# Performance work log

Measured on AMD Instinct MI355X. Metric: run time of the kernel, lower is better.

Reference implementation:

```python
import jax, jax.numpy as jnp
import numpy as np

H = W = 128; WS = 8; SHIFT = 4; HEADS = 4; T = 2; EPS = 1e-5
N = WS * WS  # tokens per window per frame


def _rel_pos_index(ws):
    ch, cw = np.meshgrid(np.arange(ws), np.arange(ws), indexing='ij')
    coords = np.stack([ch, cw]).reshape(2, -1)  # (2, N)
    rel = coords[:, :, None] - coords[:, None, :]  # (2, N, N)
    rel = rel.transpose(1, 2, 0)
    rel[:, :, 0] += ws - 1
    rel[:, :, 1] += ws - 1
    rel[:, :, 0] *= 2 * ws - 1
    return rel.sum(-1)  # (N, N) int


def _attn_mask(h, w, ws, shift):
    img = np.zeros((h, w))
    cnt = 0
    for hs in (slice(0, -ws), slice(-ws, -shift), slice(-shift, None)):
        for wsl in (slice(0, -ws), slice(-ws, -shift), slice(-shift, None)):
            img[hs, wsl] = cnt
            cnt += 1
    mw = img.reshape(h // ws, ws, w // ws, ws).transpose(0, 2, 1, 3).reshape(-1, ws * ws)
    diff = mw[:, None, :] - mw[:, :, None]
    return np.where(diff != 0, -100.0, 0.0).astype(np.float32)  # (nW, N, N)


REL_IDX = jnp.asarray(_rel_pos_index(WS))
ATTN_MASK = jnp.asarray(_attn_mask(H, W, WS, SHIFT))


def _ln(x, g, b):
    mu = x.mean(-1, keepdims=True)
    var = ((x - mu) ** 2).mean(-1, keepdims=True)
    return (x - mu) * jax.lax.rsqrt(var + EPS) * g + b


def setup_inputs() -> dict:
    key = jax.random.key(0)
    ks = jax.random.split(key, 8)
    B, C = 4, 128
    hid = 4 * C
    s = 0.02
    return {
        'x_v': jax.random.normal(ks[0], (B, T, H * W, C), jnp.float32),
        'qkv_w': jax.random.normal(ks[1], (3 * C, C), jnp.float32) * s,
        'qkv_b': jnp.zeros((3 * C,), jnp.float32),
        'proj_w': jax.random.normal(ks[2], (C, C), jnp.float32) * s,
        'proj_b': jnp.zeros((C,), jnp.float32),
        'rpb_table': jax.random.normal(ks[3], ((2 * WS - 1) ** 2, HEADS), jnp.float32) * s,
        'norm1_w': jnp.ones((C,), jnp.float32),
        'norm1_b': jnp.zeros((C,), jnp.float32),
        'norm2_w': jnp.ones((C,), jnp.float32),
        'norm2_b': jnp.zeros((C,), jnp.float32),
        'fc1_w': jax.random.normal(ks[4], (hid, C), jnp.float32) * s,
        'fc1_b': jnp.zeros((hid,), jnp.float32),
        'fc2_w': jax.random.normal(ks[5], (C, hid), jnp.float32) * s,
        'fc2_b': jnp.zeros((C,), jnp.float32),
    }


def reference(x_v, qkv_w, qkv_b, proj_w, proj_b, rpb_table,
              norm1_w, norm1_b, norm2_w, norm2_b,
              fc1_w, fc1_b, fc2_w, fc2_b):
    B, Tt, L, C = x_v.shape
    hd = C // HEADS
    nWh, nWw = H // WS, W // WS
    nW = nWh * nWw
    TN = T * N

    shortcut = x_v.reshape(B * T, L, C)
    x = x_v.reshape(B * T, H, W, C)
    x = jnp.roll(x, (-SHIFT, -SHIFT), axis=(1, 2))
    # window partition: (B*T, nWh, ws, nWw, ws, C) -> (B*nW, T, N, C)
    x = x.reshape(B * T, nWh, WS, nWw, WS, C).transpose(0, 1, 3, 2, 4, 5)
    x = x.reshape(B, T, nW, N, C).transpose(0, 2, 1, 3, 4).reshape(B * nW, T, N, C)

    # --- window attention over T*N tokens ---
    B_ = B * nW
    xf = x.reshape(B_, TN, C)
    qkv = xf @ qkv_w.T + qkv_b  # (B_, TN, 3C)
    qkv = qkv.reshape(B_, TN, 3, HEADS, hd).transpose(2, 0, 3, 1, 4)
    q, k, v = qkv[0], qkv[1], qkv[2]  # (B_, heads, TN, hd)
    q = q * (hd ** -0.5)
    attn = jnp.einsum('bhqd,bhkd->bhqk', q, k)  # (B_, heads, TN, TN)

    rpb = rpb_table[REL_IDX.reshape(-1)].reshape(N, N, HEADS).transpose(2, 0, 1)
    rpb = jnp.tile(rpb, (1, T, T))  # (heads, TN, TN)
    attn = attn + rpb[None]

    mask = jnp.tile(ATTN_MASK, (1, T, T))  # (nW, TN, TN)
    attn = attn.reshape(B, nW, HEADS, TN, TN) + mask[None, :, None]
    attn = jax.nn.softmax(attn.reshape(B_, HEADS, TN, TN), axis=-1)

    out = jnp.einsum('bhqk,bhkd->bhqd', attn, v)  # (B_, heads, TN, hd)
    out = out.transpose(0, 2, 1, 3).reshape(B_, T, N, C)
    out = out.reshape(B_ * T * N, C) @ proj_w.T + proj_b
    out = out.reshape(B_, T, N, C)

    # window reverse: (B*nW, T, N, C) -> (B, T, H, W, C)
    x = out.reshape(B, nWh, nWw, T, WS, WS, C).transpose(0, 3, 1, 4, 2, 5, 6)
    x = x.reshape(B * T, H, W, C)
    x = jnp.roll(x, (SHIFT, SHIFT), axis=(1, 2)).reshape(B * T, L, C)

    x = shortcut + x
    h = _ln(x, norm2_w, norm2_b)
    h = jax.nn.gelu(h @ fc1_w.T + fc1_b, approximate=False) @ fc2_w.T + fc2_b
    x = _ln(x + h, norm1_w, norm1_b)
    return x.reshape(B, T, L, C)
```

## Files before the change

kernel.cpp:

```cpp
#include <hip/hip_runtime.h>

typedef unsigned short us;
typedef short s16x8 __attribute__((ext_vector_type(8)));
typedef float f32x4 __attribute__((ext_vector_type(4)));

__device__ __forceinline__ us f2bf(float f) {
  union { float f; unsigned u; } v; v.f = f;
  unsigned u = v.u;
  u += 0x7fffu + ((u >> 16) & 1u);
  return (us)(u >> 16);
}
__device__ __forceinline__ float bf2f(us u) {
  union { unsigned u; float f; } v; v.u = ((unsigned)u) << 16; return v.f;
}
__device__ __forceinline__ s16x8 ld8(const us* p) { return *(const s16x8*)p; }

#define MFMA(a, b, c) __builtin_amdgcn_mfma_f32_16x16x32_bf16(a, b, c, 0, 0, 0)

__device__ __forceinline__ void lds_fence() {
  asm volatile("s_waitcnt lgkmcnt(0)" ::: "memory");
}

__device__ __forceinline__ float qsum(float v) {
  v += __shfl_xor(v, 1, 64); v += __shfl_xor(v, 2, 64);
  v += __shfl_xor(v, 4, 64); v += __shfl_xor(v, 8, 64);
  return v;
}

__device__ __forceinline__ float gelu_fast(float x) {
  float ax = fabsf(x);
  float t = __builtin_amdgcn_rcpf(1.f + 0.3275911f * ax);
  float p = t * (0.254829592f +
            t * (-0.284496736f +
            t * (1.421413741f +
            t * (-1.453152027f +
            t * 1.061405429f))));
  float e = __expf(-ax * ax);
  float er = copysignf(1.f - p * e, x);
  return 0.5f * x * (1.f + er);
}

__global__ void prep_kernel(const float* __restrict__ qkv_w, const float* __restrict__ proj_w,
                            const float* __restrict__ fc1_w, const float* __restrict__ fc2_w,
                            const float* __restrict__ rpb_table,
                            us* __restrict__ qkvw, us* __restrict__ projw,
                            us* __restrict__ fc1w, us* __restrict__ fc2w,
                            us* __restrict__ rpbm) {
  int id = blockIdx.x * 256 + threadIdx.x;
  if (id < 49152) {
    int n = id % 384, k = id / 384;
    float v = qkv_w[n * 128 + k];
    if (n < 128) v *= 0.17677669529663687f;
    qkvw[(((k >> 3) * 384 + n) << 3) + (k & 7)] = f2bf(v);
    return;
  }
  id -= 49152;
  if (id < 16384) { int n = id % 128, k = id / 128;
    projw[(((k >> 3) * 128 + n) << 3) + (k & 7)] = f2bf(proj_w[n * 128 + k]); return; }
  id -= 16384;
  if (id < 65536) { int n = id % 512, k = id / 512;
    fc1w[(((k >> 3) * 512 + n) << 3) + (k & 7)] = f2bf(fc1_w[n * 128 + k]); return; }
  id -= 65536;
  if (id < 65536) { int n = id % 128, k = id / 128;
    fc2w[(((k >> 3) * 128 + n) << 3) + (k & 7)] = f2bf(fc2_w[n * 512 + k]); return; }
  id -= 65536;
  {
    int h = id >> 14, cls = (id >> 12) & 3, e = id & 4095;
    int n1 = e >> 6, n2 = e & 63;
    int r1 = n1 >> 3, c1 = n1 & 7, r2 = n2 >> 3, c2 = n2 & 7;
    int cH = cls >> 1, cW = cls & 1;
    int cq = (cH ? (r1 < 4 ? 1 : 2) : 0) * 3 + (cW ? (c1 < 4 ? 1 : 2) : 0);
    int ck = (cH ? (r2 < 4 ? 1 : 2) : 0) * 3 + (cW ? (c2 < 4 ? 1 : 2) : 0);
    int ridx = (r1 - r2 + 7) * 15 + (c1 - c2 + 7);
    float v = rpb_table[ridx * 4 + h] + (cq != ck ? -100.f : 0.f);
    rpbm[id] = f2bf(v);
  }
}

__global__ __launch_bounds__(512, 2) void qkv_attn_kernel(
    const float* __restrict__ x_v, const us* __restrict__ qkvw,
    const float* __restrict__ qkv_b, const us* __restrict__ rpbm,
    us* __restrict__ attn_out) {
  __shared__ __align__(16) unsigned char smem[139264];
  us* A   = (us*)smem;
  us* Qs  = (us*)smem;
  us* Ks  = (us*)(smem + 34816);
  us* Vts = (us*)(smem + 69632);

  int w = blockIdx.x;
  int b = w >> 8, wi = w & 255, wh = wi >> 4, ww = wi & 15;
  int tid = threadIdx.x;

  {
    int token = tid >> 2, q = tid & 3;
    int t = token >> 6, n = token & 63, r = n >> 3, c = n & 7;
    int hs = (wh * 8 + r + 4) & 127, wsc = (ww * 8 + c + 4) & 127;
    const float* src = x_v + (size_t)((b * 2 + t) * 16384 + hs * 128 + wsc) * 128 + q * 32;
    us* dst = A + token * 136 + q * 32;
#pragma unroll
    for (int i = 0; i < 4; ++i) {
      float4 f0 = ((const float4*)src)[2 * i];
      float4 f1 = ((const float4*)src)[2 * i + 1];
      s16x8 v;
      v[0] = (short)f2bf(f0.x); v[1] = (short)f2bf(f0.y);
      v[2] = (short)f2bf(f0.z); v[3] = (short)f2bf(f0.w);
      v[4] = (short)f2bf(f1.x); v[5] = (short)f2bf(f1.y);
      v[6] = (short)f2bf(f1.z); v[7] = (short)f2bf(f1.w);
      *(s16x8*)(dst + i * 8) = v;
    }
  }
  __syncthreads();

  int lane = tid & 63, wv = tid >> 6, quad = lane >> 4, c16 = lane & 15;
  int h = wv >> 1, p = wv & 1;
  int clsid = ((wh == 15) ? 2 : 0) + ((ww == 15) ? 1 : 0);

  int rb = p * 64;
  f32x4 acc[4][6];
#pragma unroll
  for (int mi = 0; mi < 4; ++mi)
#pragma unroll
    for (int ni = 0; ni < 6; ++ni) acc[mi][ni] = (f32x4){0.f, 0.f, 0.f, 0.f};
#pragma unroll
  for (int ks = 0; ks < 4; ++ks) {
    int k0 = ks * 32;
    s16x8 af[4];
#pragma unroll
    for (int mi = 0; mi < 4; ++mi)
      af[mi] = ld8(A + (rb + mi * 16 + c16) * 136 + k0 + quad * 8);
#pragma unroll
    for (int ni = 0; ni < 6; ++ni) {
      int gcol = (ni >> 1) * 128 + h * 32 + (ni & 1) * 16 + c16;
      s16x8 bf = ld8(qkvw + ((((k0 >> 3) + quad) * 384 + gcol) << 3));
#pragma unroll
      for (int mi = 0; mi < 4; ++mi) acc[mi][ni] = MFMA(af[mi], bf, acc[mi][ni]);
    }
  }
  __syncthreads();
#pragma unroll
  for (int ni = 0; ni < 6; ++ni) {
    int part = ni >> 1, colh = (ni & 1) * 16 + c16;
    int col = h * 32 + colh;
    float bias = qkv_b[part * 128 + col];
    if (part == 0) bias *= 0.17677669529663687f;
#pragma unroll
    for (int mi = 0; mi < 4; ++mi)
#pragma unroll
      for (int r = 0; r < 4; ++r) {
        int tok = rb + mi * 16 + quad * 4 + r;
        us v = f2bf(acc[mi][ni][r] + bias);
        if (part == 0) Qs[tok * 136 + col] = v;
        else if (part == 1) Ks[tok * 136 + col] = v;
        else Vts[col * 136 + tok] = v;
      }
  }
  __syncthreads();

  us* Pw = (us*)(smem + 104448 + wv * 4352);
  const us* rsrc = rpbm + ((h * 4 + clsid) << 12);
  int cb = h * 32;

  for (int qq = 0; qq < 4; ++qq) {
    int q0 = (p * 4 + qq) * 16;
    s16x8 aq = ld8(Qs + (q0 + c16) * 136 + cb + quad * 8);
    float rbv[8][4];
#pragma unroll
    for (int nj = 0; nj < 8; ++nj) {
      int nk = (nj * 16 + c16) & 63;
#pragma unroll
      for (int r = 0; r < 4; ++r) {
        int nq = (q0 + quad * 4 + r) & 63;
        rbv[nj][r] = bf2f(rsrc[nq * 64 + nk]);
      }
    }
    f32x4 sacc[8];
#pragma unroll
    for (int nj = 0; nj < 8; ++nj) {
      s16x8 bk = ld8(Ks + (nj * 16 + c16) * 136 + cb + quad * 8);
      f32x4 z = (f32x4){0.f, 0.f, 0.f, 0.f};
      sacc[nj] = MFMA(aq, bk, z);
    }
    float sm[4] = {0.f, 0.f, 0.f, 0.f};
#pragma unroll
    for (int nj = 0; nj < 8; ++nj)
#pragma unroll
      for (int r = 0; r < 4; ++r) {
        float pp = __expf(sacc[nj][r] + rbv[nj][r]);
        sacc[nj][r] = pp;
        sm[r] += pp;
      }
    float inv[4];
#pragma unroll
    for (int r = 0; r < 4; ++r) inv[r] = 1.f / qsum(sm[r]);
#pragma unroll
    for (int nj = 0; nj < 8; ++nj)
#pragma unroll
      for (int r = 0; r < 4; ++r)
        Pw[(quad * 4 + r) * 136 + nj * 16 + c16] = f2bf(sacc[nj][r] * inv[r]);
    lds_fence();
    f32x4 oacc[2];
    oacc[0] = (f32x4){0.f, 0.f, 0.f, 0.f};
    oacc[1] = (f32x4){0.f, 0.f, 0.f, 0.f};
#pragma unroll
    for (int ks = 0; ks < 4; ++ks) {
      int k0 = ks * 32;
      s16x8 ap = ld8(Pw + c16 * 136 + k0 + quad * 8);
#pragma unroll
      for (int nt = 0; nt < 2; ++nt) {
        s16x8 bv = ld8(Vts + (cb + nt * 16 + c16) * 136 + k0 + quad * 8);
        oacc[nt] = MFMA(ap, bv, oacc[nt]);
      }
    }
#pragma unroll
    for (int nt = 0; nt < 2; ++nt)
#pragma unroll
      for (int r = 0; r < 4; ++r) {
        int tok = q0 + quad * 4 + r;
        attn_out[((size_t)w * 128 + tok) * 128 + cb + nt * 16 + c16] =
            f2bf(oacc[nt][r]);
      }
    lds_fence();
  }
}

__global__ __launch_bounds__(256) void fused_kernel5(
    const us* __restrict__ attn_ws, const us* __restrict__ projw,
    const float* __restrict__ proj_b, const float* __restrict__ x_v,
    const us* __restrict__ fc1w, const us* __restrict__ fc2w,
    const float* __restrict__ fc1_b, const float* __restrict__ fc2_b,
    const float* __restrict__ n2w, const float* __restrict__ n2b,
    const float* __restrict__ n1w, const float* __restrict__ n1b,
    float* __restrict__ out) {
  __shared__ __align__(16) unsigned char smem[26624];
  us* A = (us*)smem;
  int blk = blockIdx.x;
  int w = blk >> 1, hb = (blk & 1) * 64;
  int b = w >> 8, wi = w & 255, wh = wi >> 4, ww = wi & 15;
  int tid = threadIdx.x;
  int lane = tid & 63, wv = tid >> 6, quad = lane >> 4, c16 = lane & 15;
  int r0 = wv * 16;
  us* Hw = (us*)(smem + 17408 + wv * 2304);

  {
    int lr = r0 + (lane >> 2), q = lane & 3;
    const us* src = attn_ws + ((size_t)w * 128 + hb + lr) * 128 + q * 32;
    us* dst = A + lr * 136 + q * 32;
#pragma unroll
    for (int i = 0; i < 4; ++i) *(s16x8*)(dst + i * 8) = ld8(src + i * 8);
  }

  size_t grow[4];
  float xv[4][8];
#pragma unroll
  for (int r = 0; r < 4; ++r) {
    int tt = hb + r0 + quad * 4 + r;
    int t = tt >> 6, n = tt & 63, rr = n >> 3, cc2 = n & 7;
    int hf = (wh * 8 + rr + 4) & 127, wf = (ww * 8 + cc2 + 4) & 127;
    grow[r] = (size_t)((b * 2 + t) * 16384 + hf * 128 + wf) * 128;
#pragma unroll
    for (int ni = 0; ni < 8; ++ni) xv[r][ni] = x_v[grow[r] + ni * 16 + c16];
  }
  lds_fence();

  f32x4 y[8];
#pragma unroll
  for (int ni = 0; ni < 8; ++ni) y[ni] = (f32x4){0.f, 0.f, 0.f, 0.f};
#pragma unroll
  for (int ks = 0; ks < 4; ++ks) {
    int k0 = ks * 32;
    s16x8 af = ld8(A + (r0 + c16) * 136 + k0 + quad * 8);
#pragma unroll
    for (int ni = 0; ni < 8; ++ni) {
      s16x8 bf = ld8(projw + ((((k0 >> 3) + quad) * 128 + ni * 16 + c16) << 3));
      y[ni] = MFMA(af, bf, y[ni]);
    }
  }

  {
    float sum[4] = {0.f, 0.f, 0.f, 0.f}, sq[4] = {0.f, 0.f, 0.f, 0.f};
#pragma unroll
    for (int ni = 0; ni < 8; ++ni) {
      float pb = proj_b[ni * 16 + c16];
#pragma unroll
      for (int r = 0; r < 4; ++r) {
        float v = y[ni][r] + pb + xv[r][ni];
        y[ni][r] = v;
        sum[r] += v; sq[r] += v * v;
      }
    }
#pragma unroll
    for (int r = 0; r < 4; ++r) {
      float s = qsum(sum[r]), q = qsum(sq[r]);
      float mean = s * 0.0078125f;
      float rstd = rsqrtf(q * 0.0078125f - mean * mean + 1e-5f);
      int m = r0 + quad * 4 + r;
#pragma unroll
      for (int ni = 0; ni < 8; ++ni) {
        int col = ni * 16 + c16;
        A[m * 136 + col] = f2bf((y[ni][r] - mean) * rstd * n2w[col] + n2b[col]);
      }
    }
  }
  lds_fence();

  f32x4 o[8];
#pragma unroll
  for (int ni = 0; ni < 8; ++ni) o[ni] = (f32x4){0.f, 0.f, 0.f, 0.f};

#pragma unroll
  for (int cc = 0; cc < 8; ++cc) {
    f32x4 f[4];
#pragma unroll
    for (int ni = 0; ni < 4; ++ni) f[ni] = (f32x4){0.f, 0.f, 0.f, 0.f};
#pragma unroll
    for (int ks = 0; ks < 4; ++ks) {
      int k0 = ks * 32;
      s16x8 af = ld8(A + (r0 + c16) * 136 + k0 + quad * 8);
#pragma unroll
      for (int ni = 0; ni < 4; ++ni) {
        s16x8 bf = ld8(fc1w + ((((k0 >> 3) + quad) * 512 + cc * 64 + ni * 16 + c16) << 3));
        f[ni] = MFMA(af, bf, f[ni]);
      }
    }
#pragma unroll
    for (int ni = 0; ni < 4; ++ni) {
      float bb = fc1_b[cc * 64 + ni * 16 + c16];
#pragma unroll
      for (int r = 0; r < 4; ++r) {
        float u = f[ni][r] + bb;
        Hw[(quad * 4 + r) * 72 + ni * 16 + c16] = f2bf(gelu_fast(u));
      }
    }
    lds_fence();
#pragma unroll
    for (int ks2 = 0; ks2 < 2; ++ks2) {
      s16x8 ah = ld8(Hw + c16 * 72 + ks2 * 32 + quad * 8);
#pragma unroll
      for (int ni = 0; ni < 8; ++ni) {
        s16x8 bf = ld8(fc2w + (((cc * 8 + ks2 * 4 + quad) * 128 + ni * 16 + c16) << 3));
        o[ni] = MFMA(ah, bf, o[ni]);
      }
    }
    lds_fence();
  }

  {
    float s1[4] = {0.f, 0.f, 0.f, 0.f}, q1[4] = {0.f, 0.f, 0.f, 0.f};
#pragma unroll
    for (int ni = 0; ni < 8; ++ni) {
      float fb = fc2_b[ni * 16 + c16];
#pragma unroll
      for (int r = 0; r < 4; ++r) {
        float v = o[ni][r] + fb + y[ni][r];
        y[ni][r] = v;
        s1[r] += v; q1[r] += v * v;
      }
    }
#pragma unroll
    for (int r = 0; r < 4; ++r) {
      float s = qsum(s1[r]), q = qsum(q1[r]);
      float mean = s * 0.0078125f;
      float rstd = rsqrtf(q * 0.0078125f - mean * mean + 1e-5f);
#pragma unroll
      for (int ni = 0; ni < 8; ++ni) {
        int col = ni * 16 + c16;
        out[grow[r] + col] = (y[ni][r] - mean) * rstd * n1w[col] + n1b[col];
      }
    }
  }
}

extern "C" void kernel_launch(void* const* d_in, const int* in_sizes, int n_in,
                              void* d_out, int out_size, void* d_ws, size_t ws_size,
                              hipStream_t stream) {
  const float* x_v   = (const float*)d_in[0];
  const float* qkv_w = (const float*)d_in[1];
  const float* qkv_b = (const float*)d_in[2];
  const float* proj_w = (const float*)d_in[3];
  const float* proj_b = (const float*)d_in[4];
  const float* rpb_t = (const float*)d_in[5];
  const float* n1w = (const float*)d_in[6];
  const float* n1b = (const float*)d_in[7];
  const float* n2w = (const float*)d_in[8];
  const float* n2b = (const float*)d_in[9];
  const float* fc1_w = (const float*)d_in[10];
  const float* fc1_b = (const float*)d_in[11];
  const float* fc2_w = (const float*)d_in[12];
  const float* fc2_b = (const float*)d_in[13];

  char* ws = (char*)d_ws;
  us* qkvw    = (us*)(ws + 0);
  us* projw   = (us*)(ws + 98304);
  us* fc1w    = (us*)(ws + 131072);
  us* fc2w    = (us*)(ws + 262144);
  us* rpbm    = (us*)(ws + 393216);
  us* attn_ws = (us*)(ws + 524288);

  prep_kernel<<<1024, 256, 0, stream>>>(qkv_w, proj_w, fc1_w, fc2_w, rpb_t,
                                        qkvw, projw, fc1w, fc2w, rpbm);
  qkv_attn_kernel<<<1024, 512, 0, stream>>>(x_v, qkvw, qkv_b, rpbm, attn_ws);
  fused_kernel5<<<2048, 256, 0, stream>>>(attn_ws, projw, proj_b, x_v,
                                          fc1w, fc2w, fc1_b, fc2_b,
                                          n2w, n2b, n1w, n1b, (float*)d_out);
}
```

Before: 319.5 us.

## Double attention block threads, shrink LDS, and fold biases into MMA accumulators

The QKV+attention kernel now runs 1024 threads per window block: each wave handles 32 rows of one head. Q fragments move into registers so the P staging buffer can reuse the Q region, which cuts LDS from 136KB to 102KB. The P@V step is split into two 64-key halves with a smaller P tile, and the rpb values are held as bf16 with half as many loaded (the pattern repeats across frames). In the MLP kernel, the shortcut and projection bias seed the proj accumulator, fc1 bias seeds the fc1 accumulator, and the LN2 input seeds the fc2 accumulator, which removes separate add passes and the xv register array. The larger block with 1024-thread launch bounds may raise register pressure or cause spills.

Measured after the change: 457.8 us. 43.3% more time.

```diff
diff --git a/kernel.cpp b/kernel.cpp
--- a/kernel.cpp
+++ b/kernel.cpp
@@ -77,11 +77,11 @@
   }
 }
 
-__global__ __launch_bounds__(512, 2) void qkv_attn_kernel(
+__global__ __launch_bounds__(1024) void qkv_attn_kernel(
     const float* __restrict__ x_v, const us* __restrict__ qkvw,
     const float* __restrict__ qkv_b, const us* __restrict__ rpbm,
     us* __restrict__ attn_out) {
-  __shared__ __align__(16) unsigned char smem[139264];
+  __shared__ __align__(16) unsigned char smem[104448];
   us* A   = (us*)smem;
   us* Qs  = (us*)smem;
   us* Ks  = (us*)(smem + 34816);
@@ -92,13 +92,13 @@
   int tid = threadIdx.x;
 
   {
-    int token = tid >> 2, q = tid & 3;
-    int t = token >> 6, n = token & 63, r = n >> 3, c = n & 7;
-    int hs = (wh * 8 + r + 4) & 127, wsc = (ww * 8 + c + 4) & 127;
-    const float* src = x_v + (size_t)((b * 2 + t) * 16384 + hs * 128 + wsc) * 128 + q * 32;
-    us* dst = A + token * 136 + q * 32;
-#pragma unroll
-    for (int i = 0; i < 4; ++i) {
+    int token = tid >> 3, oct = tid & 7;
+    int t = token >> 6, n = token & 63, rr = n >> 3, cc = n & 7;
+    int hs = (wh * 8 + rr + 4) & 127, wsc = (ww * 8 + cc + 4) & 127;
+    const float* src = x_v + (size_t)((b * 2 + t) * 16384 + hs * 128 + wsc) * 128 + oct * 16;
+    us* dst = A + token * 136 + oct * 16;
+#pragma unroll
+    for (int i = 0; i < 2; ++i) {
       float4 f0 = ((const float4*)src)[2 * i];
       float4 f1 = ((const float4*)src)[2 * i + 1];
       s16x8 v;
@@ -112,39 +112,40 @@
   __syncthreads();
 
   int lane = tid & 63, wv = tid >> 6, quad = lane >> 4, c16 = lane & 15;
-  int h = wv >> 1, p = wv & 1;
+  int h = wv >> 2, rq = wv & 3;
   int clsid = ((wh == 15) ? 2 : 0) + ((ww == 15) ? 1 : 0);
-
-  int rb = p * 64;
-  f32x4 acc[4][6];
-#pragma unroll
-  for (int mi = 0; mi < 4; ++mi)
+  int cb = h * 32;
+
+  int rb = rq * 32;
+  f32x4 acc[2][6];
+#pragma unroll
+  for (int mi = 0; mi < 2; ++mi)
 #pragma unroll
     for (int ni = 0; ni < 6; ++ni) acc[mi][ni] = (f32x4){0.f, 0.f, 0.f, 0.f};
 #pragma unroll
   for (int ks = 0; ks < 4; ++ks) {
     int k0 = ks * 32;
-    s16x8 af[4];
-#pragma unroll
-    for (int mi = 0; mi < 4; ++mi)
+    s16x8 af[2];
+#pragma unroll
+    for (int mi = 0; mi < 2; ++mi)
       af[mi] = ld8(A + (rb + mi * 16 + c16) * 136 + k0 + quad * 8);
 #pragma unroll
     for (int ni = 0; ni < 6; ++ni) {
-      int gcol = (ni >> 1) * 128 + h * 32 + (ni & 1) * 16 + c16;
+      int gcol = (ni >> 1) * 128 + cb + (ni & 1) * 16 + c16;
       s16x8 bf = ld8(qkvw + ((((k0 >> 3) + quad) * 384 + gcol) << 3));
 #pragma unroll
-      for (int mi = 0; mi < 4; ++mi) acc[mi][ni] = MFMA(af[mi], bf, acc[mi][ni]);
+      for (int mi = 0; mi < 2; ++mi) acc[mi][ni] = MFMA(af[mi], bf, acc[mi][ni]);
     }
   }
   __syncthreads();
 #pragma unroll
   for (int ni = 0; ni < 6; ++ni) {
     int part = ni >> 1, colh = (ni & 1) * 16 + c16;
-    int col = h * 32 + colh;
+    int col = cb + colh;
     float bias = qkv_b[part * 128 + col];
     if (part == 0) bias *= 0.17677669529663687f;
 #pragma unroll
-    for (int mi = 0; mi < 4; ++mi)
+    for (int mi = 0; mi < 2; ++mi)
 #pragma unroll
       for (int r = 0; r < 4; ++r) {
         int tok = rb + mi * 16 + quad * 4 + r;
@@ -156,21 +157,26 @@
   }
   __syncthreads();
 
-  us* Pw = (us*)(smem + 104448 + wv * 4352);
+  s16x8 aq[2];
+#pragma unroll
+  for (int qq = 0; qq < 2; ++qq)
+    aq[qq] = ld8(Qs + (((rq * 2 + qq) * 16) + c16) * 136 + cb + quad * 8);
+  __syncthreads();
+
+  us* Pw = (us*)smem + wv * 1088;
   const us* rsrc = rpbm + ((h * 4 + clsid) << 12);
-  int cb = h * 32;
-
-  for (int qq = 0; qq < 4; ++qq) {
-    int q0 = (p * 4 + qq) * 16;
-    s16x8 aq = ld8(Qs + (q0 + c16) * 136 + cb + quad * 8);
-    float rbv[8][4];
-#pragma unroll
-    for (int nj = 0; nj < 8; ++nj) {
+
+#pragma unroll
+  for (int qq = 0; qq < 2; ++qq) {
+    int q0 = (rq * 2 + qq) * 16;
+    us rb16[4][4];
+#pragma unroll
+    for (int nj = 0; nj < 4; ++nj) {
       int nk = (nj * 16 + c16) & 63;
 #pragma unroll
       for (int r = 0; r < 4; ++r) {
         int nq = (q0 + quad * 4 + r) & 63;
-        rbv[nj][r] = bf2f(rsrc[nq * 64 + nk]);
+        rb16[nj][r] = rsrc[nq * 64 + nk];
       }
     }
     f32x4 sacc[8];
@@ -178,38 +184,43 @@
     for (int nj = 0; nj < 8; ++nj) {
       s16x8 bk = ld8(Ks + (nj * 16 + c16) * 136 + cb + quad * 8);
       f32x4 z = (f32x4){0.f, 0.f, 0.f, 0.f};
-      sacc[nj] = MFMA(aq, bk, z);
+      sacc[nj] = MFMA(aq[qq], bk, z);
     }
     float sm[4] = {0.f, 0.f, 0.f, 0.f};
 #pragma unroll
     for (int nj = 0; nj < 8; ++nj)
 #pragma unroll
       for (int r = 0; r < 4; ++r) {
-        float pp = __expf(sacc[nj][r] + rbv[nj][r]);
+        float pp = __expf(sacc[nj][r] + bf2f(rb16[nj & 3][r]));
         sacc[nj][r] = pp;
         sm[r] += pp;
       }
     float inv[4];
 #pragma unroll
     for (int r = 0; r < 4; ++r) inv[r] = 1.f / qsum(sm[r]);
-#pragma unroll
-    for (int nj = 0; nj < 8; ++nj)
-#pragma unroll
-      for (int r = 0; r < 4; ++r)
-        Pw[(quad * 4 + r) * 136 + nj * 16 + c16] = f2bf(sacc[nj][r] * inv[r]);
-    lds_fence();
+
     f32x4 oacc[2];
     oacc[0] = (f32x4){0.f, 0.f, 0.f, 0.f};
     oacc[1] = (f32x4){0.f, 0.f, 0.f, 0.f};
 #pragma unroll
-    for (int ks = 0; ks < 4; ++ks) {
-      int k0 = ks * 32;
-      s16x8 ap = ld8(Pw + c16 * 136 + k0 + quad * 8);
-#pragma unroll
-      for (int nt = 0; nt < 2; ++nt) {
-        s16x8 bv = ld8(Vts + (cb + nt * 16 + c16) * 136 + k0 + quad * 8);
-        oacc[nt] = MFMA(ap, bv, oacc[nt]);
-      }
+    for (int kh = 0; kh < 2; ++kh) {
+#pragma unroll
+      for (int njl = 0; njl < 4; ++njl)
+#pragma unroll
+        for (int r = 0; r < 4; ++r)
+          Pw[(quad * 4 + r) * 68 + njl * 16 + c16] =
+              f2bf(sacc[kh * 4 + njl][r] * inv[r]);
+      lds_fence();
+#pragma unroll
+      for (int ksl = 0; ksl < 2; ++ksl) {
+        s16x8 ap = ld8(Pw + c16 * 68 + ksl * 32 + quad * 8);
+#pragma unroll
+        for (int nt = 0; nt < 2; ++nt) {
+          s16x8 bv = ld8(Vts + (cb + nt * 16 + c16) * 136 + kh * 64 + ksl * 32 + quad * 8);
+          oacc[nt] = MFMA(ap, bv, oacc[nt]);
+        }
+      }
+      lds_fence();
     }
 #pragma unroll
     for (int nt = 0; nt < 2; ++nt)
@@ -219,7 +230,6 @@
         attn_out[((size_t)w * 128 + tok) * 128 + cb + nt * 16 + c16] =
             f2bf(oacc[nt][r]);
       }
-    lds_fence();
   }
 }
 
@@ -250,21 +260,22 @@
   }
 
   size_t grow[4];
-  float xv[4][8];
 #pragma unroll
   for (int r = 0; r < 4; ++r) {
     int tt = hb + r0 + quad * 4 + r;
     int t = tt >> 6, n = tt & 63, rr = n >> 3, cc2 = n & 7;
     int hf = (wh * 8 + rr + 4) & 127, wf = (ww * 8 + cc2 + 4) & 127;
     grow[r] = (size_t)((b * 2 + t) * 16384 + hf * 128 + wf) * 128;
-#pragma unroll
-    for (int ni = 0; ni < 8; ++ni) xv[r][ni] = x_v[grow[r] + ni * 16 + c16];
+  }
+  f32x4 y[8];
+#pragma unroll
+  for (int ni = 0; ni < 8; ++ni) {
+    float pb = proj_b[ni * 16 + c16];
+#pragma unroll
+    for (int r = 0; r < 4; ++r) y[ni][r] = x_v[grow[r] + ni * 16 + c16] + pb;
   }
   lds_fence();
 
-  f32x4 y[8];
-#pragma unroll
-  for (int ni = 0; ni < 8; ++ni) y[ni] = (f32x4){0.f, 0.f, 0.f, 0.f};
 #pragma unroll
   for (int ks = 0; ks < 4; ++ks) {
     int k0 = ks * 32;
@@ -279,15 +290,12 @@
   {
     float sum[4] = {0.f, 0.f, 0.f, 0.f}, sq[4] = {0.f, 0.f, 0.f, 0.f};
 #pragma unroll
-    for (int ni = 0; ni < 8; ++ni) {
-      float pb = proj_b[ni * 16 + c16];
-#pragma unroll
-      for (int r = 0; r < 4; ++r) {
-        float v = y[ni][r] + pb + xv[r][ni];
-        y[ni][r] = v;
+    for (int ni = 0; ni < 8; ++ni)
+#pragma unroll
+      for (int r = 0; r < 4; ++r) {
+        float v = y[ni][r];
         sum[r] += v; sq[r] += v * v;
       }
-    }
 #pragma unroll
     for (int r = 0; r < 4; ++r) {
       float s = qsum(sum[r]), q = qsum(sq[r]);
@@ -305,13 +313,16 @@
 
   f32x4 o[8];
 #pragma unroll
-  for (int ni = 0; ni < 8; ++ni) o[ni] = (f32x4){0.f, 0.f, 0.f, 0.f};
+  for (int ni = 0; ni < 8; ++ni) o[ni] = y[ni];
 
 #pragma unroll
   for (int cc = 0; cc < 8; ++cc) {
     f32x4 f[4];
 #pragma unroll
-    for (int ni = 0; ni < 4; ++ni) f[ni] = (f32x4){0.f, 0.f, 0.f, 0.f};
+    for (int ni = 0; ni < 4; ++ni) {
+      float bb = fc1_b[cc * 64 + ni * 16 + c16];
+      f[ni] = (f32x4){bb, bb, bb, bb};
+    }
 #pragma unroll
     for (int ks = 0; ks < 4; ++ks) {
       int k0 = ks * 32;
@@ -323,14 +334,10 @@
       }
     }
 #pragma unroll
-    for (int ni = 0; ni < 4; ++ni) {
-      float bb = fc1_b[cc * 64 + ni * 16 + c16];
-#pragma unroll
-      for (int r = 0; r < 4; ++r) {
-        float u = f[ni][r] + bb;
-        Hw[(quad * 4 + r) * 72 + ni * 16 + c16] = f2bf(gelu_fast(u));
-      }
-    }
+    for (int ni = 0; ni < 4; ++ni)
+#pragma unroll
+      for (int r = 0; r < 4; ++r)
+        Hw[(quad * 4 + r) * 72 + ni * 16 + c16] = f2bf(gelu_fast(f[ni][r]));
     lds_fence();
 #pragma unroll
     for (int ks2 = 0; ks2 < 2; ++ks2) {
@@ -351,8 +358,8 @@
       float fb = fc2_b[ni * 16 + c16];
 #pragma unroll
       for (int r = 0; r < 4; ++r) {
-        float v = o[ni][r] + fb + y[ni][r];
-        y[ni][r] = v;
+        float v = o[ni][r] + fb;
+        o[ni][r] = v;
         s1[r] += v; q1[r] += v * v;
       }
     }
@@ -364,7 +371,7 @@
 #pragma unroll
       for (int ni = 0; ni < 8; ++ni) {
         int col = ni * 16 + c16;
-        out[grow[r] + col] = (y[ni][r] - mean) * rstd * n1w[col] + n1b[col];
+        out[grow[r] + col] = (o[ni][r] - mean) * rstd * n1w[col] + n1b[col];
       }
     }
   }
@@ -398,7 +405,7 @@
 
   prep_kernel<<<1024, 256, 0, stream>>>(qkv_w, proj_w, fc1_w, fc2_w, rpb_t,
                                         qkvw, projw, fc1w, fc2w, rpbm);
-  qkv_attn_kernel<<<1024, 512, 0, stream>>>(x_v, qkvw, qkv_b, rpbm, attn_ws);
+  qkv_attn_kernel<<<1024, 1024, 0, stream>>>(x_v, qkvw, qkv_b, rpbm, attn_ws);
   fused_kernel5<<<2048, 256, 0, stream>>>(attn_ws, projw, proj_b, x_v,
                                           fc1w, fc2w, fc1_b, fc2_b,
                                           n2w, n2b, n1w, n1b, (float*)d_out);
```

## Stage fc1/fc2 weight chunks in LDS shared across waves in MLP kernel

Applied to the files above, without the earlier changes.

The fused proj+MLP kernel now copies each 64-column chunk of fc1 and fc2 weights into padded LDS buffers cooperatively, once per block, instead of every wave loading the same weight fragments from global memory. fc1 weights are re-laid out in the prep kernel so each chunk is contiguous. This cuts redundant global/L2 traffic four-fold, but it raises LDS use to about 58KB per block, which lowers occupancy. It also adds block-wide barriers per chunk with no double buffering, and the chunk loop is no longer unrolled.

Result: faster. 286.6 us (-10.3%).

```diff
diff --git a/kernel.cpp b/kernel.cpp
--- a/kernel.cpp
+++ b/kernel.cpp
@@ -59,7 +59,8 @@
     projw[(((k >> 3) * 128 + n) << 3) + (k & 7)] = f2bf(proj_w[n * 128 + k]); return; }
   id -= 16384;
   if (id < 65536) { int n = id % 512, k = id / 512;
-    fc1w[(((k >> 3) * 512 + n) << 3) + (k & 7)] = f2bf(fc1_w[n * 128 + k]); return; }
+    fc1w[((n >> 6) * 16 + (k >> 3)) * 512 + (n & 63) * 8 + (k & 7)] = f2bf(fc1_w[n * 128 + k]);
+    return; }
   id -= 65536;
   if (id < 65536) { int n = id % 128, k = id / 128;
     fc2w[(((k >> 3) * 128 + n) << 3) + (k & 7)] = f2bf(fc2_w[n * 512 + k]); return; }
@@ -223,7 +224,7 @@
   }
 }
 
-__global__ __launch_bounds__(256) void fused_kernel5(
+__global__ __launch_bounds__(256) void fused_kernel6(
     const us* __restrict__ attn_ws, const us* __restrict__ projw,
     const float* __restrict__ proj_b, const float* __restrict__ x_v,
     const us* __restrict__ fc1w, const us* __restrict__ fc2w,
@@ -231,15 +232,17 @@
     const float* __restrict__ n2w, const float* __restrict__ n2b,
     const float* __restrict__ n1w, const float* __restrict__ n1b,
     float* __restrict__ out) {
-  __shared__ __align__(16) unsigned char smem[26624];
-  us* A = (us*)smem;
+  __shared__ __align__(16) unsigned char smem[59776];
+  us* A   = (us*)smem;
+  us* Ws1 = (us*)(smem + 17408);
+  us* Ws2 = (us*)(smem + 34048);
   int blk = blockIdx.x;
   int w = blk >> 1, hb = (blk & 1) * 64;
   int b = w >> 8, wi = w & 255, wh = wi >> 4, ww = wi & 15;
   int tid = threadIdx.x;
   int lane = tid & 63, wv = tid >> 6, quad = lane >> 4, c16 = lane & 15;
   int r0 = wv * 16;
-  us* Hw = (us*)(smem + 17408 + wv * 2304);
+  us* Hw = (us*)(smem + 50560 + wv * 2304);
 
   {
     int lr = r0 + (lane >> 2), q = lane & 3;
@@ -260,6 +263,23 @@
 #pragma unroll
     for (int ni = 0; ni < 8; ++ni) xv[r][ni] = x_v[grow[r] + ni * 16 + c16];
   }
+
+  {
+#pragma unroll
+    for (int i = 0; i < 4; ++i) {
+      int j = wv * 4 + i;
+      s16x8 t = ld8(fc1w + j * 512 + lane * 8);
+      *(s16x8*)(Ws1 + j * 520 + lane * 8) = t;
+    }
+#pragma unroll
+    for (int i = 0; i < 2; ++i) {
+      int j = wv * 2 + i;
+      s16x8 t0 = ld8(fc2w + j * 1024 + lane * 8);
+      s16x8 t1 = ld8(fc2w + j * 1024 + 512 + lane * 8);
+      *(s16x8*)(Ws2 + j * 1032 + lane * 8) = t0;
+      *(s16x8*)(Ws2 + j * 1032 + 512 + lane * 8) = t1;
+    }
+  }
   lds_fence();
 
   f32x4 y[8];
@@ -307,8 +327,8 @@
 #pragma unroll
   for (int ni = 0; ni < 8; ++ni) o[ni] = (f32x4){0.f, 0.f, 0.f, 0.f};
 
-#pragma unroll
   for (int cc = 0; cc < 8; ++cc) {
+    __syncthreads();
     f32x4 f[4];
 #pragma unroll
     for (int ni = 0; ni < 4; ++ni) f[ni] = (f32x4){0.f, 0.f, 0.f, 0.f};
@@ -318,7 +338,7 @@
       s16x8 af = ld8(A + (r0 + c16) * 136 + k0 + quad * 8);
 #pragma unroll
       for (int ni = 0; ni < 4; ++ni) {
-        s16x8 bf = ld8(fc1w + ((((k0 >> 3) + quad) * 512 + cc * 64 + ni * 16 + c16) << 3));
+        s16x8 bf = ld8(Ws1 + (ks * 4 + quad) * 520 + (ni * 16 + c16) * 8);
         f[ni] = MFMA(af, bf, f[ni]);
       }
     }
@@ -337,11 +357,30 @@
       s16x8 ah = ld8(Hw + c16 * 72 + ks2 * 32 + quad * 8);
 #pragma unroll
       for (int ni = 0; ni < 8; ++ni) {
-        s16x8 bf = ld8(fc2w + (((cc * 8 + ks2 * 4 + quad) * 128 + ni * 16 + c16) << 3));
+        s16x8 bf = ld8(Ws2 + (ks2 * 4 + quad) * 1032 + (ni * 16 + c16) * 8);
         o[ni] = MFMA(ah, bf, o[ni]);
       }
     }
-    lds_fence();
+    if (cc < 7) {
+      __syncthreads();
+      int cn = cc + 1;
+#pragma unroll
+      for (int i = 0; i < 4; ++i) {
+        int j = wv * 4 + i;
+        s16x8 t = ld8(fc1w + (cn * 16 + j) * 512 + lane * 8);
+        *(s16x8*)(Ws1 + j * 520 + lane * 8) = t;
+      }
+#pragma unroll
+      for (int i = 0; i < 2; ++i) {
+        int j = wv * 2 + i;
+        s16x8 t0 = ld8(fc2w + cn * 8192 + j * 1024 + lane * 8);
+        s16x8 t1 = ld8(fc2w + cn * 8192 + j * 1024 + 512 + lane * 8);
+        *(s16x8*)(Ws2 + j * 1032 + lane * 8) = t0;
+        *(s16x8*)(Ws2 + j * 1032 + 512 + lane * 8) = t1;
+      }
+    } else {
+      lds_fence();
+    }
   }
 
   {
@@ -399,7 +438,7 @@
   prep_kernel<<<1024, 256, 0, stream>>>(qkv_w, proj_w, fc1_w, fc2_w, rpb_t,
                                         qkvw, projw, fc1w, fc2w, rpbm);
   qkv_attn_kernel<<<1024, 512, 0, stream>>>(x_v, qkvw, qkv_b, rpbm, attn_ws);
-  fused_kernel5<<<2048, 256, 0, stream>>>(attn_ws, projw, proj_b, x_v,
+  fused_kernel6<<<2048, 256, 0, stream>>>(attn_ws, projw, proj_b, x_v,
                                           fc1w, fc2w, fc1_b, fc2_b,
                                           n2w, n2b, n1w, n1b, (float*)d_out);
 }
```

## Stage MLP weight chunks in LDS, hoist LN tile loads, use tanh-form GELU

Applied to the files above, without the earlier changes.

The fc1/fc2 weights are re-laid out in the prep kernel into per-chunk contiguous tiles. Each block now copies each 16 KB chunk into LDS cooperatively and reads MFMA B operands from LDS instead of global memory. The normalized A fragments are hoisted into registers ahead of the chunk loop, and the erf-based GELU becomes a cheaper sigmoid/tanh approximation. LDS use per block grows from about 26 KB to about 58 KB, which lowers occupancy and adds barriers; the GELU approximation also changes numerics slightly.

Result: faster. 273.4 us (-14.4%).

```diff
diff --git a/kernel.cpp b/kernel.cpp
--- a/kernel.cpp
+++ b/kernel.cpp
@@ -28,16 +28,10 @@
 }
 
 __device__ __forceinline__ float gelu_fast(float x) {
-  float ax = fabsf(x);
-  float t = __builtin_amdgcn_rcpf(1.f + 0.3275911f * ax);
-  float p = t * (0.254829592f +
-            t * (-0.284496736f +
-            t * (1.421413741f +
-            t * (-1.453152027f +
-            t * 1.061405429f))));
-  float e = __expf(-ax * ax);
-  float er = copysignf(1.f - p * e, x);
-  return 0.5f * x * (1.f + er);
+  float x2 = x * x;
+  float nz = x * (-1.5957691216f - 0.0713548163f * x2);
+  float e = __expf(nz);
+  return x * __builtin_amdgcn_rcpf(1.f + e);
 }
 
 __global__ void prep_kernel(const float* __restrict__ qkv_w, const float* __restrict__ proj_w,
@@ -58,11 +52,19 @@
   if (id < 16384) { int n = id % 128, k = id / 128;
     projw[(((k >> 3) * 128 + n) << 3) + (k & 7)] = f2bf(proj_w[n * 128 + k]); return; }
   id -= 16384;
-  if (id < 65536) { int n = id % 512, k = id / 512;
-    fc1w[(((k >> 3) * 512 + n) << 3) + (k & 7)] = f2bf(fc1_w[n * 128 + k]); return; }
+  if (id < 65536) {
+    int n = id % 512, k = id / 512;
+    int cc = n >> 6, ni = (n >> 4) & 3, c16v = n & 15;
+    int ks = k >> 5, qd = (k >> 3) & 3, j = k & 7;
+    fc1w[cc * 8192 + (ks * 4 + ni) * 512 + (qd * 16 + c16v) * 8 + j] = f2bf(fc1_w[n * 128 + k]);
+    return; }
   id -= 65536;
-  if (id < 65536) { int n = id % 128, k = id / 128;
-    fc2w[(((k >> 3) * 128 + n) << 3) + (k & 7)] = f2bf(fc2_w[n * 512 + k]); return; }
+  if (id < 65536) {
+    int n = id % 128, k = id / 128;
+    int cc = k >> 6, ks2 = (k >> 5) & 1, qd = (k >> 3) & 3, j = k & 7;
+    int ni = n >> 4, c16v = n & 15;
+    fc2w[cc * 8192 + (ks2 * 8 + ni) * 512 + (qd * 16 + c16v) * 8 + j] = f2bf(fc2_w[n * 512 + k]);
+    return; }
   id -= 65536;
   {
     int h = id >> 14, cls = (id >> 12) & 3, e = id & 4095;
@@ -223,7 +225,7 @@
   }
 }
 
-__global__ __launch_bounds__(256) void fused_kernel5(
+__global__ __launch_bounds__(256) void fused_kernel7(
     const us* __restrict__ attn_ws, const us* __restrict__ projw,
     const float* __restrict__ proj_b, const float* __restrict__ x_v,
     const us* __restrict__ fc1w, const us* __restrict__ fc2w,
@@ -231,15 +233,17 @@
     const float* __restrict__ n2w, const float* __restrict__ n2b,
     const float* __restrict__ n1w, const float* __restrict__ n1b,
     float* __restrict__ out) {
-  __shared__ __align__(16) unsigned char smem[26624];
-  us* A = (us*)smem;
+  __shared__ __align__(16) unsigned char smem[59392];
+  us* A   = (us*)smem;
+  us* Ws1 = (us*)(smem + 17408);
+  us* Ws2 = (us*)(smem + 33792);
   int blk = blockIdx.x;
   int w = blk >> 1, hb = (blk & 1) * 64;
   int b = w >> 8, wi = w & 255, wh = wi >> 4, ww = wi & 15;
   int tid = threadIdx.x;
   int lane = tid & 63, wv = tid >> 6, quad = lane >> 4, c16 = lane & 15;
   int r0 = wv * 16;
-  us* Hw = (us*)(smem + 17408 + wv * 2304);
+  us* Hw = (us*)(smem + 50176 + wv * 2304);
 
   {
     int lr = r0 + (lane >> 2), q = lane & 3;
@@ -260,6 +264,17 @@
 #pragma unroll
     for (int ni = 0; ni < 8; ++ni) xv[r][ni] = x_v[grow[r] + ni * 16 + c16];
   }
+
+  {
+    const s16x8* s1 = (const s16x8*)fc1w;
+    const s16x8* s2 = (const s16x8*)fc2w;
+    s16x8* d1 = (s16x8*)Ws1;
+    s16x8* d2 = (s16x8*)Ws2;
+#pragma unroll
+    for (int i = 0; i < 4; ++i) d1[i * 256 + tid] = s1[i * 256 + tid];
+#pragma unroll
+    for (int i = 0; i < 4; ++i) d2[i * 256 + tid] = s2[i * 256 + tid];
+  }
   lds_fence();
 
   f32x4 y[8];
@@ -303,25 +318,27 @@
   }
   lds_fence();
 
+  s16x8 afm[4];
+#pragma unroll
+  for (int ks = 0; ks < 4; ++ks)
+    afm[ks] = ld8(A + (r0 + c16) * 136 + ks * 32 + quad * 8);
+
   f32x4 o[8];
 #pragma unroll
   for (int ni = 0; ni < 8; ++ni) o[ni] = (f32x4){0.f, 0.f, 0.f, 0.f};
 
-#pragma unroll
   for (int cc = 0; cc < 8; ++cc) {
+    __syncthreads();
     f32x4 f[4];
 #pragma unroll
     for (int ni = 0; ni < 4; ++ni) f[ni] = (f32x4){0.f, 0.f, 0.f, 0.f};
 #pragma unroll
-    for (int ks = 0; ks < 4; ++ks) {
-      int k0 = ks * 32;
-      s16x8 af = ld8(A + (r0 + c16) * 136 + k0 + quad * 8);
+    for (int ks = 0; ks < 4; ++ks)
 #pragma unroll
       for (int ni = 0; ni < 4; ++ni) {
-        s16x8 bf = ld8(fc1w + ((((k0 >> 3) + quad) * 512 + cc * 64 + ni * 16 + c16) << 3));
-        f[ni] = MFMA(af, bf, f[ni]);
-      }
-    }
+        s16x8 bf = ld8(Ws1 + (ks * 4 + ni) * 512 + lane * 8);
+        f[ni] = MFMA(afm[ks], bf, f[ni]);
+      }
 #pragma unroll
     for (int ni = 0; ni < 4; ++ni) {
       float bb = fc1_b[cc * 64 + ni * 16 + c16];
@@ -337,15 +354,28 @@
       s16x8 ah = ld8(Hw + c16 * 72 + ks2 * 32 + quad * 8);
 #pragma unroll
       for (int ni = 0; ni < 8; ++ni) {
-        s16x8 bf = ld8(fc2w + (((cc * 8 + ks2 * 4 + quad) * 128 + ni * 16 + c16) << 3));
+        s16x8 bf = ld8(Ws2 + (ks2 * 8 + ni) * 512 + lane * 8);
         o[ni] = MFMA(ah, bf, o[ni]);
       }
     }
-    lds_fence();
-  }
-
-  {
-    float s1[4] = {0.f, 0.f, 0.f, 0.f}, q1[4] = {0.f, 0.f, 0.f, 0.f};
+    if (cc < 7) {
+      __syncthreads();
+      int cn = cc + 1;
+      const s16x8* s1 = (const s16x8*)fc1w + cn * 1024;
+      const s16x8* s2 = (const s16x8*)fc2w + cn * 1024;
+      s16x8* d1 = (s16x8*)Ws1;
+      s16x8* d2 = (s16x8*)Ws2;
+#pragma unroll
+      for (int i = 0; i < 4; ++i) d1[i * 256 + tid] = s1[i * 256 + tid];
+#pragma unroll
+      for (int i = 0; i < 4; ++i) d2[i * 256 + tid] = s2[i * 256 + tid];
+    } else {
+      lds_fence();
+    }
+  }
+
+  {
+    float s1v[4] = {0.f, 0.f, 0.f, 0.f}, q1[4] = {0.f, 0.f, 0.f, 0.f};
 #pragma unroll
     for (int ni = 0; ni < 8; ++ni) {
       float fb = fc2_b[ni * 16 + c16];
@@ -353,12 +383,12 @@
       for (int r = 0; r < 4; ++r) {
         float v = o[ni][r] + fb + y[ni][r];
         y[ni][r] = v;
-        s1[r] += v; q1[r] += v * v;
+        s1v[r] += v; q1[r] += v * v;
       }
     }
 #pragma unroll
     for (int r = 0; r < 4; ++r) {
-      float s = qsum(s1[r]), q = qsum(q1[r]);
+      float s = qsum(s1v[r]), q = qsum(q1[r]);
       float mean = s * 0.0078125f;
       float rstd = rsqrtf(q * 0.0078125f - mean * mean + 1e-5f);
 #pragma unroll
@@ -399,7 +429,7 @@
   prep_kernel<<<1024, 256, 0, stream>>>(qkv_w, proj_w, fc1_w, fc2_w, rpb_t,
                                         qkvw, projw, fc1w, fc2w, rpbm);
   qkv_attn_kernel<<<1024, 512, 0, stream>>>(x_v, qkvw, qkv_b, rpbm, attn_ws);
-  fused_kernel5<<<2048, 256, 0, stream>>>(attn_ws, projw, proj_b, x_v,
+  fused_kernel7<<<2048, 256, 0, stream>>>(attn_ws, projw, proj_b, x_v,
                                           fc1w, fc2w, fc1_b, fc2_b,
                                           n2w, n2b, n1w, n1b, (float*)d_out);
 }
```
